# Kernel optimization log

Measured on AMD Instinct MI355X. Metric: run time of the kernel, lower is better.

## Reference

```python
import jax, jax.numpy as jnp
import numpy as np

SIZE = 8192
M = 1024


def logmatexp(A, B):
    # out[i, j] = logsumexp_k(A[i, k] + B[k, j]), computed stably without
    # materializing the [n, n, m] broadcast tensor:
    # log(exp(A - rowmax_A) @ exp(B - colmax_B)) + rowmax_A + colmax_B
    mA = jnp.max(A, axis=1, keepdims=True)   # [n, 1]
    mB = jnp.max(B, axis=0, keepdims=True)   # [1, m]
    return jnp.log(jnp.exp(A - mA) @ jnp.exp(B - mB)) + mA + mB


def setup_inputs() -> dict:
    key = jax.random.key(0)
    x = jax.random.normal(key, (SIZE, M), dtype=jnp.float32)
    diag = jnp.ones((SIZE,), dtype=jnp.float32)  # nn.Parameter init: ones
    return {"x": x, "diag": diag}


def reference(x, diag):
    # Faithful to forward(): logmatexp(torch.diag(self.diag), x)
    D = jnp.diag(diag)  # dense [SIZE, SIZE], zeros off-diagonal
    return logmatexp(D, x)
```

## Files before the change

### kernel.cpp

```cpp
#include <hip/hip_runtime.h>
#include <math.h>

#define N_ROWS 8192
#define N_COLS 1024

__global__ __launch_bounds__(1024) void colsum_part(
    const float* __restrict__ x, float* __restrict__ ps) {
    const int b    = blockIdx.x;
    const int t    = threadIdx.x;
    const int col0 = (t & 255) * 4;
    const int rg   = t >> 8;
    const int row0 = b * 32 + rg * 8;

    float4 s4 = make_float4(0.f, 0.f, 0.f, 0.f);
#pragma unroll
    for (int k = 0; k < 8; ++k) {
        const float4 v = *reinterpret_cast<const float4*>(
            x + (size_t)(row0 + k) * N_COLS + col0);
        s4.x += __expf(v.x); s4.y += __expf(v.y);
        s4.z += __expf(v.z); s4.w += __expf(v.w);
    }

    __shared__ float red[4][N_COLS];
    *reinterpret_cast<float4*>(&red[rg][col0]) = s4;
    __syncthreads();
    ps[(size_t)b * N_COLS + t] = red[0][t] + red[1][t] + red[2][t] + red[3][t];
}

__global__ __launch_bounds__(1024) void merge_finalize(
    const float* __restrict__ x, const float* __restrict__ diag,
    const float* __restrict__ ps, float* __restrict__ out) {
    const int cs = blockIdx.x & 3;
    const int rb = blockIdx.x >> 2;
    const int c0 = cs * 256;
    const int t  = threadIdx.x;

    __shared__ float red[4][256];
    __shared__ float S[256];
    {
        const int cg = t >> 8;
        const int c  = t & 255;
        float s = 0.f;
#pragma unroll 8
        for (int k = 0; k < 64; ++k)
            s += ps[(size_t)(cg * 64 + k) * N_COLS + c0 + c];
        red[cg][c] = s;
    }
    __syncthreads();
    if (t < 256) S[t] = red[0][t] + red[1][t] + red[2][t] + red[3][t];
    __syncthreads();

    const int lane = t & 63;
    const int w    = t >> 6;
    const int r0   = rb * 128 + w * 8;
    const float4 Sj = *reinterpret_cast<const float4*>(&S[4 * lane]);

#pragma unroll
    for (int k = 0; k < 8; ++k) {
        const int row = r0 + k;
        const float E = __expf(diag[row]) - 1.f;
        const size_t off = (size_t)row * N_COLS + c0 + 4 * lane;
        const float4 v = *reinterpret_cast<const float4*>(x + off);
        float4 o;
        o.x = __logf(fmaf(E, __expf(v.x), Sj.x));
        o.y = __logf(fmaf(E, __expf(v.y), Sj.y));
        o.z = __logf(fmaf(E, __expf(v.z), Sj.z));
        o.w = __logf(fmaf(E, __expf(v.w), Sj.w));
        *reinterpret_cast<float4*>(out + off) = o;
    }
}

extern "C" void kernel_launch(void* const* d_in, const int* in_sizes, int n_in,
                              void* d_out, int out_size, void* d_ws, size_t ws_size,
                              hipStream_t stream) {
    const float* x    = (const float*)d_in[0];
    const float* diag = (const float*)d_in[1];
    float* out = (float*)d_out;
    float* ps  = (float*)d_ws;

    colsum_part<<<256, 1024, 0, stream>>>(x, ps);
    merge_finalize<<<256, 1024, 0, stream>>>(x, diag, ps, out);
}
```

Measured before the change: 26.56 us.

## Fuse column-sum and finalize into one cooperative kernel caching exp(x) in LDS

Replaces the two-kernel pipeline with a single cooperative kernel. Each block computes exp(x) for its 32 rows, keeps it in 128KB of shared memory, and writes partial column sums. Two grid-wide syncs then reduce the column sums, and the finalize step reads the cached exp values instead of reloading x from global memory. This is meant to remove the second pass over x and one kernel launch, at the cost of grid.sync overhead and large LDS usage that limits occupancy to one block per CU. If the cooperative launch fails, it falls back to the original two kernels.

```diff
diff --git a/kernel.cpp b/kernel.cpp
--- a/kernel.cpp
+++ b/kernel.cpp
@@ -1,8 +1,90 @@
 #include <hip/hip_runtime.h>
+#include <hip/hip_cooperative_groups.h>
 #include <math.h>
+
+namespace cg = cooperative_groups;
 
 #define N_ROWS 8192
 #define N_COLS 1024
+#define NBLK   256
+#define NTHR   1024
+#define RPB    32
+
+__global__ __launch_bounds__(NTHR, 4) void fused_logmatexp(
+    const float* __restrict__ x, const float* __restrict__ diag,
+    float* __restrict__ ps,
+    float* __restrict__ S,
+    float* __restrict__ out)
+{
+    cg::grid_group grid = cg::this_grid();
+    __shared__ float ex[RPB][N_COLS];
+    __shared__ float red[4][N_COLS];
+    __shared__ float redS[16];
+
+    const int t    = threadIdx.x;
+    const int b    = blockIdx.x;
+    const int col0 = (t & 255) * 4;
+    const int rg   = t >> 8;
+    const int r0   = rg * 8;
+    const int row0 = b * RPB + r0;
+
+    float4 s4 = make_float4(0.f, 0.f, 0.f, 0.f);
+#pragma unroll
+    for (int k = 0; k < 8; ++k) {
+        const float4 v = *reinterpret_cast<const float4*>(
+            x + (size_t)(row0 + k) * N_COLS + col0);
+        float4 e;
+        e.x = __expf(v.x); e.y = __expf(v.y);
+        e.z = __expf(v.z); e.w = __expf(v.w);
+        *reinterpret_cast<float4*>(&ex[r0 + k][col0]) = e;
+        s4.x += e.x; s4.y += e.y; s4.z += e.z; s4.w += e.w;
+    }
+    *reinterpret_cast<float4*>(&red[rg][col0]) = s4;
+    __syncthreads();
+    if (t < 256) {
+        float4 a = *reinterpret_cast<const float4*>(&red[0][col0]);
+        const float4 b1 = *reinterpret_cast<const float4*>(&red[1][col0]);
+        const float4 b2 = *reinterpret_cast<const float4*>(&red[2][col0]);
+        const float4 b3 = *reinterpret_cast<const float4*>(&red[3][col0]);
+        a.x += b1.x + b2.x + b3.x;  a.y += b1.y + b2.y + b3.y;
+        a.z += b1.z + b2.z + b3.z;  a.w += b1.w + b2.w + b3.w;
+        *reinterpret_cast<float4*>(ps + (size_t)b * N_COLS + col0) = a;
+    }
+
+    grid.sync();
+
+    {
+        const int g    = t >> 8;
+        const int sub  = t & 255;
+        const int col  = b * 4 + g;
+        const int lane = t & 63;
+        const int wid  = t >> 6;
+        float s = ps[(size_t)sub * N_COLS + col];
+#pragma unroll
+        for (int off = 32; off; off >>= 1) s += __shfl_down(s, off);
+        if (lane == 0) redS[wid] = s;
+        __syncthreads();
+        if (sub == 0)
+            S[col] = redS[4 * g + 0] + redS[4 * g + 1] +
+                     redS[4 * g + 2] + redS[4 * g + 3];
+    }
+
+    grid.sync();
+
+    const float4 Sj = *reinterpret_cast<const float4*>(S + col0);
+#pragma unroll
+    for (int k = 0; k < 8; ++k) {
+        const int row = row0 + k;
+        const float E = __expf(diag[row]) - 1.f;
+        const float4 e = *reinterpret_cast<const float4*>(&ex[r0 + k][col0]);
+        float4 o;
+        o.x = __logf(fmaf(E, e.x, Sj.x));
+        o.y = __logf(fmaf(E, e.y, Sj.y));
+        o.z = __logf(fmaf(E, e.z, Sj.z));
+        o.w = __logf(fmaf(E, e.w, Sj.w));
+        *reinterpret_cast<float4*>(out + (size_t)row * N_COLS + col0) = o;
+    }
+}
 
 __global__ __launch_bounds__(1024) void colsum_part(
     const float* __restrict__ x, float* __restrict__ ps) {
@@ -20,7 +102,6 @@
         s4.x += __expf(v.x); s4.y += __expf(v.y);
         s4.z += __expf(v.z); s4.w += __expf(v.w);
     }
-
     __shared__ float red[4][N_COLS];
     *reinterpret_cast<float4*>(&red[rg][col0]) = s4;
     __syncthreads();
@@ -76,8 +157,16 @@
     const float* x    = (const float*)d_in[0];
     const float* diag = (const float*)d_in[1];
     float* out = (float*)d_out;
-    float* ps  = (float*)d_ws;
+    float* ws  = (float*)d_ws;
 
-    colsum_part<<<256, 1024, 0, stream>>>(x, ps);
-    merge_finalize<<<256, 1024, 0, stream>>>(x, diag, ps, out);
+    float* ps = ws;
+    float* S  = ps + NBLK * N_COLS;
+
+    void* args[] = { (void*)&x, (void*)&diag, (void*)&ps, (void*)&S, (void*)&out };
+    hipError_t err = hipLaunchCooperativeKernel((const void*)fused_logmatexp,
+                                                dim3(NBLK), dim3(NTHR), args, 0, stream);
+    if (err != hipSuccess) {
+        colsum_part<<<256, 1024, 0, stream>>>(x, ps);
+        merge_finalize<<<256, 1024, 0, stream>>>(x, diag, ps, out);
+    }
 }
```

Measured after the change: 81.43 us. 207% more time.

## Replace partial-sum buffer with atomic column sums and simplify finalize

Applied to the files above, without the earlier changes.

Each colsum block now atomically adds its 1024 column sums into a single global vector instead of writing a 256x1024 partial buffer. The finalize kernel no longer re-reduces 64 partial rows per block and just reads the final sums, which removes about 1 MB of partial-sum traffic and a block-level reduction. In exchange it adds a memset launch and 262K float atomics that contend on 1024 addresses. Floating-point summation order also becomes nondeterministic.

```diff
diff --git a/kernel.cpp b/kernel.cpp
--- a/kernel.cpp
+++ b/kernel.cpp
@@ -4,8 +4,8 @@
 #define N_ROWS 8192
 #define N_COLS 1024
 
-__global__ __launch_bounds__(1024) void colsum_part(
-    const float* __restrict__ x, float* __restrict__ ps) {
+__global__ __launch_bounds__(1024) void colsum_atomic(
+    const float* __restrict__ x, float* __restrict__ S) {
     const int b    = blockIdx.x;
     const int t    = threadIdx.x;
     const int col0 = (t & 255) * 4;
@@ -24,42 +24,26 @@
     __shared__ float red[4][N_COLS];
     *reinterpret_cast<float4*>(&red[rg][col0]) = s4;
     __syncthreads();
-    ps[(size_t)b * N_COLS + t] = red[0][t] + red[1][t] + red[2][t] + red[3][t];
+    const float s = red[0][t] + red[1][t] + red[2][t] + red[3][t];
+    atomicAdd(&S[t], s);
 }
 
-__global__ __launch_bounds__(1024) void merge_finalize(
+__global__ __launch_bounds__(1024) void finalize_stream(
     const float* __restrict__ x, const float* __restrict__ diag,
-    const float* __restrict__ ps, float* __restrict__ out) {
-    const int cs = blockIdx.x & 3;
-    const int rb = blockIdx.x >> 2;
-    const int c0 = cs * 256;
-    const int t  = threadIdx.x;
+    const float* __restrict__ S, float* __restrict__ out) {
+    const int b    = blockIdx.x;
+    const int t    = threadIdx.x;
+    const int col0 = (t & 255) * 4;
+    const int rg   = t >> 8;
+    const int row0 = b * 32 + rg * 8;
 
-    __shared__ float red[4][256];
-    __shared__ float S[256];
-    {
-        const int cg = t >> 8;
-        const int c  = t & 255;
-        float s = 0.f;
-#pragma unroll 8
-        for (int k = 0; k < 64; ++k)
-            s += ps[(size_t)(cg * 64 + k) * N_COLS + c0 + c];
-        red[cg][c] = s;
-    }
-    __syncthreads();
-    if (t < 256) S[t] = red[0][t] + red[1][t] + red[2][t] + red[3][t];
-    __syncthreads();
-
-    const int lane = t & 63;
-    const int w    = t >> 6;
-    const int r0   = rb * 128 + w * 8;
-    const float4 Sj = *reinterpret_cast<const float4*>(&S[4 * lane]);
+    const float4 Sj = *reinterpret_cast<const float4*>(S + col0);
 
 #pragma unroll
     for (int k = 0; k < 8; ++k) {
-        const int row = r0 + k;
+        const int row = row0 + k;
         const float E = __expf(diag[row]) - 1.f;
-        const size_t off = (size_t)row * N_COLS + c0 + 4 * lane;
+        const size_t off = (size_t)row * N_COLS + col0;
         const float4 v = *reinterpret_cast<const float4*>(x + off);
         float4 o;
         o.x = __logf(fmaf(E, __expf(v.x), Sj.x));
@@ -76,8 +60,9 @@
     const float* x    = (const float*)d_in[0];
     const float* diag = (const float*)d_in[1];
     float* out = (float*)d_out;
-    float* ps  = (float*)d_ws;
+    float* S   = (float*)d_ws;
 
-    colsum_part<<<256, 1024, 0, stream>>>(x, ps);
-    merge_finalize<<<256, 1024, 0, stream>>>(x, diag, ps, out);
+    hipMemsetAsync(S, 0, N_COLS * sizeof(float), stream);
+    colsum_atomic<<<256, 1024, 0, stream>>>(x, S);
+    finalize_stream<<<256, 1024, 0, stream>>>(x, diag, S, out);
 }
```

After: 30.05 us. 13.1% more time.
